# Optimization experiments

Hardware: AMD Instinct MI355X
Metric: run time of the kernel (lower is better)

The kernel has to match this reference:

```python
import jax, jax.numpy as jnp
import numpy as np

SIGMA_COLOR = 0.05
WINDOW_SIZE = 5


def setup_inputs() -> dict:
    key = jax.random.key(0)
    k1, k2 = jax.random.split(key)
    preds = jax.random.normal(k1, (4, 21, 512, 512), dtype=jnp.float32)
    images = jax.random.uniform(k2, (4, 3, 512, 512), dtype=jnp.float32)
    return {"preds": preds, "images": images}


def reference(preds, images):
    # preds: [B, C, H, W] logits; images: [B, 3, H, W]
    B, C, H, W = preds.shape
    pad = WINDOW_SIZE // 2
    inv_two_sigma2 = 1.0 / (2.0 * SIGMA_COLOR ** 2)

    probs = jax.nn.softmax(preds, axis=1)
    pad_cfg = ((0, 0), (0, 0), (pad, pad), (pad, pad))
    probs_padded = jnp.pad(probs, pad_cfg, mode="reflect")
    img_padded = jnp.pad(images, pad_cfg, mode="reflect")

    loss = jnp.zeros((), dtype=preds.dtype)
    count = 0
    for dy in range(-pad, pad + 1):
        for dx in range(-pad, pad + 1):
            if dx == 0 and dy == 0:
                continue
            sp = probs_padded[:, :, pad + dy:pad + dy + H, pad + dx:pad + dx + W]
            si = img_padded[:, :, pad + dy:pad + dy + H, pad + dx:pad + dx + W]
            color_diff = ((images - si) ** 2).sum(axis=1, keepdims=True)  # [B,1,H,W]
            affinity = jnp.exp(-color_diff * inv_two_sigma2)             # [B,1,H,W]
            diff = (probs - sp) ** 2                                     # [B,C,H,W]
            # sum_c mean_{B,H,W}(aff * diff_c) == mean_{B,H,W}(aff * sum_c diff_c)
            loss = loss + (affinity * diff).sum(axis=1).mean()
            count += 1
    return loss / (count * C)
```

## Files before the change

kernel.cpp:

```cpp
#include <hip/hip_runtime.h>
#include <hip/hip_fp16.h>

#define HH 512
#define WW 512
#define BB 4
#define CC 21
#define HWP (HH * WW)
#define TSX 64
#define TSY 16
#define HSY (TSY + 2)
#define HSX (TSX + 4)
#define PADX 2
#define NTHR 1024
#define NBLK ((WW / TSX) * (HH / TSY) * BB)

typedef _Float16 h2 __attribute__((ext_vector_type(2)));

__device__ __forceinline__ int refl(int i, int n) {
    if (i < 0) i = -i;
    if (i >= n) i = 2 * n - 2 - i;
    return i;
}

__device__ __forceinline__ float dot2(unsigned int a, unsigned int b, float c) {
#if __has_builtin(__builtin_amdgcn_fdot2)
    return __builtin_amdgcn_fdot2(__builtin_bit_cast(h2, a), __builtin_bit_cast(h2, b), c, false);
#else
    h2 ha = __builtin_bit_cast(h2, a), hb = __builtin_bit_cast(h2, b);
    return c + (float)ha[0] * (float)hb[0] + (float)ha[1] * (float)hb[1];
#endif
}

__device__ __forceinline__ unsigned int pkrtz(float a, float b) {
    return __builtin_bit_cast(unsigned int, __builtin_amdgcn_cvt_pkrtz(a, b));
}

__device__ __forceinline__ float hi_half(unsigned int u) {
    return (float)__builtin_bit_cast(h2, u)[1];
}

__global__ void zero_kernel(float* o) { *o = 0.0f; }

__global__ __launch_bounds__(NTHR, 8) void lnc_kernel(const float* __restrict__ preds,
                                                      const float* __restrict__ images,
                                                      float* __restrict__ out) {
    __shared__ uint4 sP[3][HSY * HSX];
    __shared__ float4 sI[HSY * HSX];
    __shared__ float sRed[NTHR / 64];

    const int id = blockIdx.x;
    const int swz = (id & 7) * (NBLK / 8) + (id >> 3);
    const int b = swz >> 8;
    const int rem = swz & 255;
    const int tyb = rem >> 3;
    const int txb = rem & 7;
    const int bx0 = txb * TSX;
    const int by0 = tyb * TSY;
    const int t = threadIdx.x;

    for (int h = t; h < HSY * HSX; h += NTHR) {
        const int hy = h / HSX, hx = h - hy * HSX;
        const int gy = refl(by0 + hy, HH);
        const int gx = refl(bx0 + hx - PADX, WW);
        const float* pb = preds + (size_t)b * CC * HWP + (size_t)gy * WW + gx;
        float v[CC];
#pragma unroll
        for (int c = 0; c < CC; ++c) v[c] = pb[(size_t)c * HWP];
        float sA = 0.0f, sB = 0.0f;
#pragma unroll
        for (int c = 0; c < CC; ++c) {
            v[c] = __expf(v[c]);
            if (c & 1) sB += v[c]; else sA += v[c];
        }
        const float inv = 1.0f / (sA + sB);
        float s2A = 0.0f, s2B = 0.0f;
#pragma unroll
        for (int c = 0; c < CC; ++c) {
            v[c] *= inv;
            if (c & 1) s2B = fmaf(v[c], v[c], s2B); else s2A = fmaf(v[c], v[c], s2A);
        }
        const float s2 = s2A + s2B;
        uint4 w0, w1, w2;
        w0.x = pkrtz(v[0], v[1]);   w0.y = pkrtz(v[2], v[3]);
        w0.z = pkrtz(v[4], v[5]);   w0.w = pkrtz(v[6], v[7]);
        w1.x = pkrtz(v[8], v[9]);   w1.y = pkrtz(v[10], v[11]);
        w1.z = pkrtz(v[12], v[13]); w1.w = pkrtz(v[14], v[15]);
        w2.x = pkrtz(v[16], v[17]); w2.y = pkrtz(v[18], v[19]);
        w2.z = pkrtz(v[20], s2);
        w2.w = 0u;
        sP[0][h] = w0;
        sP[1][h] = w1;
        sP[2][h] = w2;
        const float* ib = images + (size_t)b * 3 * HWP + (size_t)gy * WW + gx;
        sI[h] = make_float4(ib[0], ib[HWP], ib[2 * HWP], 0.0f);
    }
    __syncthreads();

    const int tx = t & (TSX - 1);
    const int ty = t >> 6;
    const int base = ty * HSX + (tx + PADX);
    const uint4 a0 = sP[0][base];
    const uint4 a1 = sP[1][base];
    const uint4 a2 = sP[2][base];
    const float4 ai = sI[base];
    const float S2p = hi_half(a2.z);

    const int OFF[12] = {
        0 * HSX + 1, 0 * HSX + 2,
        1 * HSX - 2, 1 * HSX - 1, 1 * HSX + 0, 1 * HSX + 1, 1 * HSX + 2,
        2 * HSX - 2, 2 * HSX - 1, 2 * HSX + 0, 2 * HSX + 1, 2 * HSX + 2};

    float accA = 0.0f, accB = 0.0f;
#pragma unroll
    for (int k = 0; k < 12; ++k) {
        const int nb = base + OFF[k];
        const uint4 q0 = sP[0][nb];
        const uint4 q1 = sP[1][nb];
        const uint4 q2 = sP[2][nb];
        const float4 qi = sI[nb];
        float d0 = 0.0f, d1 = 0.0f, d2 = 0.0f, d3 = 0.0f;
        d0 = dot2(a0.x, q0.x, d0); d1 = dot2(a0.y, q0.y, d1);
        d2 = dot2(a0.z, q0.z, d2); d3 = dot2(a0.w, q0.w, d3);
        d0 = dot2(a1.x, q1.x, d0); d1 = dot2(a1.y, q1.y, d1);
        d2 = dot2(a1.z, q1.z, d2); d3 = dot2(a1.w, q1.w, d3);
        d0 = dot2(a2.x, q2.x, d0); d1 = dot2(a2.y, q2.y, d1);
        d2 = dot2(a2.z, q2.z, d2); d3 = dot2(a2.w, q2.w, d3);
        const float dotFull = (d0 + d1) + (d2 + d3);
        const float S2q = hi_half(q2.z);
        const float ssd = fmaf(2.0f * S2p, S2q, S2p + S2q) - 2.0f * dotFull;
        const float dr = ai.x - qi.x;
        const float dg = ai.y - qi.y;
        const float db = ai.z - qi.z;
        const float cd = dr * dr + dg * dg + db * db;
        const float aff = __expf(-200.0f * cd);
        if (k & 1) accB = fmaf(aff, ssd, accB); else accA = fmaf(aff, ssd, accA);
    }
    float acc = accA + accB;

#pragma unroll
    for (int o = 32; o >= 1; o >>= 1) acc += __shfl_xor(acc, o, 64);
    if ((t & 63) == 0) sRed[t >> 6] = acc;
    __syncthreads();
    if (t == 0) {
        float tot = 0.0f;
#pragma unroll
        for (int i = 0; i < NTHR / 64; ++i) tot += sRed[i];
        constexpr float SCALE = (float)(2.0 / (504.0 * 1048576.0));
        atomicAdd(out, tot * SCALE);
    }
}

extern "C" void kernel_launch(void* const* d_in, const int* in_sizes, int n_in,
                              void* d_out, int out_size, void* d_ws, size_t ws_size,
                              hipStream_t stream) {
    const float* preds = (const float*)d_in[0];
    const float* images = (const float*)d_in[1];
    float* out = (float*)d_out;
    zero_kernel<<<1, 1, 0, stream>>>(out);
    lnc_kernel<<<NBLK, NTHR, 0, stream>>>(preds, images, out);
}
```

Measured before the change: 40.20 us.

## Process two pixels per thread and pack image colors into fp16 LDS slots

Each thread now computes two vertically adjacent pixels, keeping both in registers and sharing each neighbour LDS fetch between them, with block size halved. Image RGB is packed as fp16 into the spare slots of the probability vector so the dot2 chain also carries color, and the color contribution is subtracted afterwards. Halo staging is restructured so interior pixels are staged directly by their owners. This reduces LDS traffic and redundant loads, but lowers color precision to fp16 and raises register use.

```diff
diff --git a/kernel.cpp b/kernel.cpp
--- a/kernel.cpp
+++ b/kernel.cpp
@@ -10,8 +10,7 @@
 #define TSY 16
 #define HSY (TSY + 2)
 #define HSX (TSX + 4)
-#define PADX 2
-#define NTHR 1024
+#define NTHR 512
 #define NBLK ((WW / TSX) * (HH / TSY) * BB)
 
 typedef _Float16 h2 __attribute__((ext_vector_type(2)));
@@ -35,17 +34,85 @@
     return __builtin_bit_cast(unsigned int, __builtin_amdgcn_cvt_pkrtz(a, b));
 }
 
-__device__ __forceinline__ float hi_half(unsigned int u) {
-    return (float)__builtin_bit_cast(h2, u)[1];
-}
+struct Px {
+    uint4 w0, w1, w2;
+    float r, g, b, s2;
+};
 
 __global__ void zero_kernel(float* o) { *o = 0.0f; }
 
-__global__ __launch_bounds__(NTHR, 8) void lnc_kernel(const float* __restrict__ preds,
+__device__ __forceinline__ void stage_px(const float* __restrict__ preds,
+                                         const float* __restrict__ images,
+                                         int b, int gy, int gx, int h,
+                                         uint4* __restrict__ sP0, uint4* __restrict__ sP1,
+                                         uint4* __restrict__ sP2, float* __restrict__ sS2,
+                                         Px& px) {
+    const float* pb = preds + (size_t)b * CC * HWP + (size_t)gy * WW + gx;
+    float v[CC];
+#pragma unroll
+    for (int c = 0; c < CC; ++c) v[c] = pb[(size_t)c * HWP];
+    float sA = 0.0f, sB = 0.0f;
+#pragma unroll
+    for (int c = 0; c < CC; ++c) {
+        v[c] = __expf(v[c]);
+        if (c & 1) sB += v[c]; else sA += v[c];
+    }
+    const float inv = 1.0f / (sA + sB);
+    float s2A = 0.0f, s2B = 0.0f;
+#pragma unroll
+    for (int c = 0; c < CC; ++c) {
+        v[c] *= inv;
+        if (c & 1) s2B = fmaf(v[c], v[c], s2B); else s2A = fmaf(v[c], v[c], s2A);
+    }
+    px.s2 = s2A + s2B;
+    const float* ib = images + (size_t)b * 3 * HWP + (size_t)gy * WW + gx;
+    const float ir = ib[0], ig = ib[HWP], ibv = ib[2 * HWP];
+    px.w0.x = pkrtz(v[0], v[1]);   px.w0.y = pkrtz(v[2], v[3]);
+    px.w0.z = pkrtz(v[4], v[5]);   px.w0.w = pkrtz(v[6], v[7]);
+    px.w1.x = pkrtz(v[8], v[9]);   px.w1.y = pkrtz(v[10], v[11]);
+    px.w1.z = pkrtz(v[12], v[13]); px.w1.w = pkrtz(v[14], v[15]);
+    px.w2.x = pkrtz(v[16], v[17]); px.w2.y = pkrtz(v[18], v[19]);
+    px.w2.z = pkrtz(v[20], ir);
+    px.w2.w = pkrtz(ig, ibv);
+    px.r = (float)__builtin_bit_cast(h2, px.w2.z)[1];
+    px.g = (float)__builtin_bit_cast(h2, px.w2.w)[0];
+    px.b = (float)__builtin_bit_cast(h2, px.w2.w)[1];
+    sP0[h] = px.w0; sP1[h] = px.w1; sP2[h] = px.w2; sS2[h] = px.s2;
+}
+
+__device__ __forceinline__ float dotAll(const Px& p, const uint4& q0, const uint4& q1,
+                                        const uint4& q2) {
+    float d0 = 0.0f, d1 = 0.0f, d2 = 0.0f, d3 = 0.0f;
+    d0 = dot2(p.w0.x, q0.x, d0); d1 = dot2(p.w0.y, q0.y, d1);
+    d2 = dot2(p.w0.z, q0.z, d2); d3 = dot2(p.w0.w, q0.w, d3);
+    d0 = dot2(p.w1.x, q1.x, d0); d1 = dot2(p.w1.y, q1.y, d1);
+    d2 = dot2(p.w1.z, q1.z, d2); d3 = dot2(p.w1.w, q1.w, d3);
+    d0 = dot2(p.w2.x, q2.x, d0); d1 = dot2(p.w2.y, q2.y, d1);
+    d2 = dot2(p.w2.z, q2.z, d2); d3 = dot2(p.w2.w, q2.w, d3);
+    return (d0 + d1) + (d2 + d3);
+}
+
+__device__ __forceinline__ float term(const Px& p, const uint4& q0, const uint4& q1,
+                                      const uint4& q2, float rq, float gq, float bq,
+                                      float s2q) {
+    const float da = dotAll(p, q0, q1, q2);
+    float dot21 = da;
+    dot21 = fmaf(-p.r, rq, dot21);
+    dot21 = fmaf(-p.g, gq, dot21);
+    dot21 = fmaf(-p.b, bq, dot21);
+    const float ssd = p.s2 + s2q - 2.0f * dot21;
+    const float dr = p.r - rq, dg = p.g - gq, db = p.b - bq;
+    const float cd = fmaf(dr, dr, fmaf(dg, dg, db * db));
+    return __expf(-200.0f * cd) * ssd;
+}
+
+__global__ __launch_bounds__(NTHR, 4) void lnc_kernel(const float* __restrict__ preds,
                                                       const float* __restrict__ images,
                                                       float* __restrict__ out) {
-    __shared__ uint4 sP[3][HSY * HSX];
-    __shared__ float4 sI[HSY * HSX];
+    __shared__ uint4 sP0[HSY * HSX];
+    __shared__ uint4 sP1[HSY * HSX];
+    __shared__ uint4 sP2[HSY * HSX];
+    __shared__ float sS2[HSY * HSX];
     __shared__ float sRed[NTHR / 64];
 
     const int id = blockIdx.x;
@@ -57,85 +124,61 @@
     const int bx0 = txb * TSX;
     const int by0 = tyb * TSY;
     const int t = threadIdx.x;
-
-    for (int h = t; h < HSY * HSX; h += NTHR) {
-        const int hy = h / HSX, hx = h - hy * HSX;
-        const int gy = refl(by0 + hy, HH);
-        const int gx = refl(bx0 + hx - PADX, WW);
-        const float* pb = preds + (size_t)b * CC * HWP + (size_t)gy * WW + gx;
-        float v[CC];
-#pragma unroll
-        for (int c = 0; c < CC; ++c) v[c] = pb[(size_t)c * HWP];
-        float sA = 0.0f, sB = 0.0f;
-#pragma unroll
-        for (int c = 0; c < CC; ++c) {
-            v[c] = __expf(v[c]);
-            if (c & 1) sB += v[c]; else sA += v[c];
+    const int tx = t & 63;
+    const int tyy = t >> 6;
+
+    Px p0, p1;
+    {
+        const int hy0 = 2 * tyy;
+        const int gy0 = by0 + hy0;
+        const int gx = bx0 + tx;
+        stage_px(preds, images, b, gy0, gx, hy0 * HSX + tx + 2, sP0, sP1, sP2, sS2, p0);
+        stage_px(preds, images, b, gy0 + 1, gx, (hy0 + 1) * HSX + tx + 2, sP0, sP1, sP2, sS2, p1);
+        if (t < 200) {
+            int r, c;
+            if (t < 136) { r = 16 + (t >= 68 ? 1 : 0); c = t - (t >= 68 ? 68 : 0); }
+            else { const int idx = t - 136; r = idx >> 2; const int c4 = idx & 3;
+                   c = (c4 < 2) ? c4 : c4 + 64; }
+            Px dummy;
+            stage_px(preds, images, b, refl(by0 + r, HH), refl(bx0 + c - 2, WW),
+                     r * HSX + c, sP0, sP1, sP2, sS2, dummy);
         }
-        const float inv = 1.0f / (sA + sB);
-        float s2A = 0.0f, s2B = 0.0f;
-#pragma unroll
-        for (int c = 0; c < CC; ++c) {
-            v[c] *= inv;
-            if (c & 1) s2B = fmaf(v[c], v[c], s2B); else s2A = fmaf(v[c], v[c], s2A);
-        }
-        const float s2 = s2A + s2B;
-        uint4 w0, w1, w2;
-        w0.x = pkrtz(v[0], v[1]);   w0.y = pkrtz(v[2], v[3]);
-        w0.z = pkrtz(v[4], v[5]);   w0.w = pkrtz(v[6], v[7]);
-        w1.x = pkrtz(v[8], v[9]);   w1.y = pkrtz(v[10], v[11]);
-        w1.z = pkrtz(v[12], v[13]); w1.w = pkrtz(v[14], v[15]);
-        w2.x = pkrtz(v[16], v[17]); w2.y = pkrtz(v[18], v[19]);
-        w2.z = pkrtz(v[20], s2);
-        w2.w = 0u;
-        sP[0][h] = w0;
-        sP[1][h] = w1;
-        sP[2][h] = w2;
-        const float* ib = images + (size_t)b * 3 * HWP + (size_t)gy * WW + gx;
-        sI[h] = make_float4(ib[0], ib[HWP], ib[2 * HWP], 0.0f);
     }
     __syncthreads();
 
-    const int tx = t & (TSX - 1);
-    const int ty = t >> 6;
-    const int base = ty * HSX + (tx + PADX);
-    const uint4 a0 = sP[0][base];
-    const uint4 a1 = sP[1][base];
-    const uint4 a2 = sP[2][base];
-    const float4 ai = sI[base];
-    const float S2p = hi_half(a2.z);
-
-    const int OFF[12] = {
-        0 * HSX + 1, 0 * HSX + 2,
-        1 * HSX - 2, 1 * HSX - 1, 1 * HSX + 0, 1 * HSX + 1, 1 * HSX + 2,
-        2 * HSX - 2, 2 * HSX - 1, 2 * HSX + 0, 2 * HSX + 1, 2 * HSX + 2};
-
-    float accA = 0.0f, accB = 0.0f;
-#pragma unroll
-    for (int k = 0; k < 12; ++k) {
-        const int nb = base + OFF[k];
-        const uint4 q0 = sP[0][nb];
-        const uint4 q1 = sP[1][nb];
-        const uint4 q2 = sP[2][nb];
-        const float4 qi = sI[nb];
-        float d0 = 0.0f, d1 = 0.0f, d2 = 0.0f, d3 = 0.0f;
-        d0 = dot2(a0.x, q0.x, d0); d1 = dot2(a0.y, q0.y, d1);
-        d2 = dot2(a0.z, q0.z, d2); d3 = dot2(a0.w, q0.w, d3);
-        d0 = dot2(a1.x, q1.x, d0); d1 = dot2(a1.y, q1.y, d1);
-        d2 = dot2(a1.z, q1.z, d2); d3 = dot2(a1.w, q1.w, d3);
-        d0 = dot2(a2.x, q2.x, d0); d1 = dot2(a2.y, q2.y, d1);
-        d2 = dot2(a2.z, q2.z, d2); d3 = dot2(a2.w, q2.w, d3);
-        const float dotFull = (d0 + d1) + (d2 + d3);
-        const float S2q = hi_half(q2.z);
-        const float ssd = fmaf(2.0f * S2p, S2q, S2p + S2q) - 2.0f * dotFull;
-        const float dr = ai.x - qi.x;
-        const float dg = ai.y - qi.y;
-        const float db = ai.z - qi.z;
-        const float cd = dr * dr + dg * dg + db * db;
-        const float aff = __expf(-200.0f * cd);
-        if (k & 1) accB = fmaf(aff, ssd, accB); else accA = fmaf(aff, ssd, accA);
-    }
-    float acc = accA + accB;
+    const int base = (2 * tyy) * HSX + (tx + 2);
+    float acc = 0.0f;
+
+    {
+        float rq = p1.r, gq = p1.g, bq = p1.b;
+        acc += term(p0, p1.w0, p1.w1, p1.w2, rq, gq, bq, p1.s2);
+    }
+
+    struct NBo { int off; bool u0, u1; };
+    constexpr NBo nbs[16] = {
+        {1, true, false},            {2, true, false},
+        {HSX - 2, true, false},      {HSX - 1, true, false},
+        {HSX + 1, true, true},       {HSX + 2, true, true},
+        {2 * HSX - 2, true, true},   {2 * HSX - 1, true, true},
+        {2 * HSX + 0, true, true},   {2 * HSX + 1, true, true},
+        {2 * HSX + 2, true, true},
+        {3 * HSX - 2, false, true},  {3 * HSX - 1, false, true},
+        {3 * HSX + 0, false, true},  {3 * HSX + 1, false, true},
+        {3 * HSX + 2, false, true}};
+
+#pragma unroll
+    for (int k = 0; k < 16; ++k) {
+        const int nb = base + nbs[k].off;
+        const uint4 q0 = sP0[nb];
+        const uint4 q1 = sP1[nb];
+        const uint4 q2 = sP2[nb];
+        const float s2q = sS2[nb];
+        const float rq = (float)__builtin_bit_cast(h2, q2.z)[1];
+        const float gq = (float)__builtin_bit_cast(h2, q2.w)[0];
+        const float bq = (float)__builtin_bit_cast(h2, q2.w)[1];
+        if (nbs[k].u0) acc += term(p0, q0, q1, q2, rq, gq, bq, s2q);
+        if (nbs[k].u1) acc += term(p1, q0, q1, q2, rq, gq, bq, s2q);
+    }
 
 #pragma unroll
     for (int o = 32; o >= 1; o >>= 1) acc += __shfl_xor(acc, o, 64);
```

Result: slower. 42.04 us (+4.6%).
